# Performance work log

Measured on AMD Instinct MI355X. Metric: run time of the kernel, lower is better.

Reference implementation:

```python
import jax, jax.numpy as jnp
import numpy as np

ALPHA = 0.2  # LeakyReLU slope
S1, S2 = 5, 10  # neighbor sample sizes, hard-coded in the torch forward

N, F, D, C, B = 100000, 512, 256, 40, 16384


def setup_inputs() -> dict:
    key = jax.random.key(0)
    ks = jax.random.split(key, 7)
    x = jax.random.normal(ks[0], (N, F), dtype=jnp.float32)
    # xavier-like scaling for the weights
    W1 = jax.random.normal(ks[1], (D, F), dtype=jnp.float32) * (2.0 / (D + F)) ** 0.5
    W2 = jax.random.normal(ks[2], (D, D), dtype=jnp.float32) * (2.0 / (D + D)) ** 0.5
    Wc = jax.random.normal(ks[3], (C, D), dtype=jnp.float32) * (2.0 / (C + D)) ** 0.5
    nodes = jax.random.randint(ks[4], (B,), 0, N, dtype=jnp.int32)
    neigh1 = jax.random.randint(ks[5], (N, S1), 0, N, dtype=jnp.int32)
    neigh2 = jax.random.randint(ks[6], (B, S2), 0, N, dtype=jnp.int32)
    return {"x": x, "W1": W1, "W2": W2, "Wc": Wc,
            "nodes": nodes, "neigh1": neigh1, "neigh2": neigh2}


def leaky_relu(v):
    return jnp.where(v >= 0, v, ALPHA * v)


def reference(x, W1, W2, Wc, nodes, neigh1, neigh2):
    # Layer 1 (MeanAggregator, gcn=True): mean over sampled neighbors + self,
    # then linear transform + LeakyReLU. Computed for all N nodes.
    agg1 = (x[neigh1].sum(axis=1) + x) / (S1 + 1)          # [N, F]
    h1 = leaky_relu(agg1 @ W1.T)                            # [N, D]
    # Layer 2: mean over sampled neighbors + self, on batch nodes.
    agg2 = (h1[neigh2].sum(axis=1) + h1[nodes]) / (S2 + 1)  # [B, D]
    h2 = leaky_relu(agg2 @ W2.T)                            # [B, D]
    # scores = self.weight.mm(x_2.t()).t()
    scores = h2 @ Wc.T                                      # [B, C]
    return scores
```

## Files before the change

kernel.cpp:

```cpp
#include <hip/hip_runtime.h>
#include <hip/hip_bf16.h>


#define NN 100000
#define FF 512
#define DD 256
#define BB 16384
#define CC 40

typedef __attribute__((ext_vector_type(8))) short bf16x8;
typedef __attribute__((ext_vector_type(4))) float f32x4;
typedef unsigned short u16;
typedef unsigned int u32;

__device__ __forceinline__ float bf_lo(u32 u) { u32 v = u << 16; float f; __builtin_memcpy(&f, &v, 4); return f; }
__device__ __forceinline__ float bf_hi(u32 u) { u32 v = u & 0xffff0000u; float f; __builtin_memcpy(&f, &v, 4); return f; }
__device__ __forceinline__ float2 bf2f(u32 u) { return make_float2(bf_lo(u), bf_hi(u)); }
__device__ __forceinline__ u32 packbf2(float a, float b) {
  __hip_bfloat162 h = __float22bfloat162_rn(make_float2(a, b));
  u32 u; __builtin_memcpy(&u, &h, 4); return u;
}
__device__ __forceinline__ u16 fbits(float v) {
  __hip_bfloat16 h = __float2bfloat16(v);
  u16 u; __builtin_memcpy(&u, &h, 2); return u;
}
__device__ __forceinline__ float lrelu(float v) { return v >= 0.f ? v : 0.2f * v; }
__device__ __forceinline__ int swz(int r, int c) { return r * 128 + ((c ^ (r & 7)) << 4); }

__global__ __launch_bounds__(256) void k0_cvt(
    const float* __restrict__ W1, const float* __restrict__ W2, const float* __restrict__ Wc,
    u16* __restrict__ w1b, u16* __restrict__ w2b, u16* __restrict__ wcb)
{
  const int i = blockIdx.x * 256 + threadIdx.x;
  const float* src; u16* dst; int off;
  if (i < 32768)      { src = W1; dst = w1b; off = i * 4; }
  else if (i < 49152) { src = W2; dst = w2b; off = (i - 32768) * 4; }
  else if (i < 51712) { src = Wc; dst = wcb; off = (i - 49152) * 4; }
  else return;
  const float4 v = *(const float4*)(src + off);
  uint2 o; o.x = packbf2(v.x, v.y); o.y = packbf2(v.z, v.w);
  *(uint2*)(dst + off) = o;
}

__global__ __launch_bounds__(512) void k1_gemm(
    const float* __restrict__ x, const u16* __restrict__ w1b, u16* __restrict__ z)
{
  __shared__ __align__(16) unsigned char lds[49152];

  const int t = threadIdx.x;
  const int rowBase = blockIdx.x * 128;
  const int lane = t & 63, w = t >> 6;
  const int wm = w >> 2, wn = w & 3;
  const int lr = lane & 15, kg = lane >> 4;

  u32 offA[2]; int aW[2];
#pragma unroll
  for (int i = 0; i < 2; ++i) {
    const int id = t + i * 512;
    const int r = id >> 3, c = id & 7;
    int row = rowBase + r; if (row > NN - 1) row = NN - 1;
    offA[i] = (u32)row * FF + c * 8;
    aW[i] = swz(r, c);
  }
  u32 offB[4]; int bW[4];
#pragma unroll
  for (int i = 0; i < 4; ++i) {
    const int id = t + i * 512;
    const int r = id >> 3, c = id & 7;
    offB[i] = (u32)r * FF + c * 8;
    bW[i] = 16384 + swz(r, c);
  }
  int aA[2][4], bA[2][4];
#pragma unroll
  for (int kk = 0; kk < 2; ++kk) {
    const int cb = kk * 4 + kg;
#pragma unroll
    for (int m = 0; m < 4; ++m) aA[kk][m] = swz(wm * 64 + m * 16 + lr, cb);
#pragma unroll
    for (int n = 0; n < 4; ++n) bA[kk][n] = 16384 + swz(wn * 64 + n * 16 + lr, cb);
  }

  f32x4 acc[4][4];
#pragma unroll
  for (int m = 0; m < 4; ++m)
#pragma unroll
    for (int n = 0; n < 4; ++n) acc[m][n] = (f32x4)0.0f;

  for (int ks = 0; ks < 8; ++ks) {
    __syncthreads();
#pragma unroll
    for (int i = 0; i < 2; ++i) {
      const float4 v0 = *(const float4*)(x + offA[i] + ks * 64);
      const float4 v1 = *(const float4*)(x + offA[i] + ks * 64 + 4);
      uint4 o;
      o.x = packbf2(v0.x, v0.y); o.y = packbf2(v0.z, v0.w);
      o.z = packbf2(v1.x, v1.y); o.w = packbf2(v1.z, v1.w);
      *(uint4*)(lds + aW[i]) = o;
    }
#pragma unroll
    for (int i = 0; i < 4; ++i)
      *(uint4*)(lds + bW[i]) = *(const uint4*)(w1b + offB[i] + ks * 64);
    __syncthreads();
#pragma unroll
    for (int kk = 0; kk < 2; ++kk) {
      bf16x8 av[4], bv[4];
#pragma unroll
      for (int m = 0; m < 4; ++m) av[m] = *(const bf16x8*)(lds + aA[kk][m]);
#pragma unroll
      for (int n = 0; n < 4; ++n) bv[n] = *(const bf16x8*)(lds + bA[kk][n]);
#pragma unroll
      for (int m = 0; m < 4; ++m)
#pragma unroll
        for (int n = 0; n < 4; ++n)
          acc[m][n] = __builtin_amdgcn_mfma_f32_16x16x32_bf16(av[m], bv[n], acc[m][n], 0, 0, 0);
    }
  }
#pragma unroll
  for (int m = 0; m < 4; ++m) {
    const int r0 = rowBase + wm * 64 + m * 16 + kg * 4;
#pragma unroll
    for (int j = 0; j < 4; ++j)
#pragma unroll
      for (int n = 0; n < 4; ++n)
        z[(u32)(r0 + j) * DD + wn * 64 + n * 16 + lr] = fbits(acc[m][n][j]);
  }
}

__global__ __launch_bounds__(256) void k2_agg1(
    const u16* __restrict__ z, const int* __restrict__ neigh1, u16* __restrict__ h1)
{
  const int t = threadIdx.x;
  const int row = blockIdx.x * 8 + (t >> 5);
  const int ch = t & 31;
  const u32 o0 = (u32)row * DD + ch * 8;
  uint4 a = *(const uint4*)(z + o0);
  float2 s0 = bf2f(a.x), s1 = bf2f(a.y), s2 = bf2f(a.z), s3 = bf2f(a.w);
#pragma unroll
  for (int j = 0; j < 5; ++j) {
    const int idx = neigh1[row * 5 + j];
    const uint4 v = *(const uint4*)(z + (u32)idx * DD + ch * 8);
    s0.x += bf_lo(v.x); s0.y += bf_hi(v.x);
    s1.x += bf_lo(v.y); s1.y += bf_hi(v.y);
    s2.x += bf_lo(v.z); s2.y += bf_hi(v.z);
    s3.x += bf_lo(v.w); s3.y += bf_hi(v.w);
  }
  const float sc = 1.0f / 6.0f;
  uint4 o;
  o.x = packbf2(lrelu(s0.x * sc), lrelu(s0.y * sc));
  o.y = packbf2(lrelu(s1.x * sc), lrelu(s1.y * sc));
  o.z = packbf2(lrelu(s2.x * sc), lrelu(s2.y * sc));
  o.w = packbf2(lrelu(s3.x * sc), lrelu(s3.y * sc));
  *(uint4*)(h1 + o0) = o;
}

__global__ __launch_bounds__(256) void k3_agg_gemm(
    const u16* __restrict__ h1, const u16* __restrict__ w2b,
    const int* __restrict__ nodes, const int* __restrict__ neigh2,
    u16* __restrict__ h2)
{
  __shared__ __align__(16) unsigned char lds[8192 + 32768];

  const int t = threadIdx.x;
  const int rowBase = blockIdx.x * 64;
  const int lane = t & 63, w = t >> 6;
  const int lr = lane & 15, kg = lane >> 4;

  u32 offA[2][11]; int aW[2];
#pragma unroll
  for (int i = 0; i < 2; ++i) {
    const int id = t + i * 256;
    const int r = id >> 3, c = id & 7;
    const int b = rowBase + r;
    offA[i][0] = (u32)nodes[b] * DD + c * 8;
#pragma unroll
    for (int j = 0; j < 10; ++j)
      offA[i][1 + j] = (u32)neigh2[b * 10 + j] * DD + c * 8;
    aW[i] = swz(r, c);
  }
  u32 offB[8]; int bW[8];
#pragma unroll
  for (int i = 0; i < 8; ++i) {
    const int id = t + i * 256;
    const int r = id >> 3, c = id & 7;
    offB[i] = (u32)r * DD + c * 8;
    bW[i] = 8192 + swz(r, c);
  }
  int aA[2][4], bA[2][4];
#pragma unroll
  for (int kk = 0; kk < 2; ++kk) {
    const int cb = kk * 4 + kg;
#pragma unroll
    for (int m = 0; m < 4; ++m) aA[kk][m] = swz(m * 16 + lr, cb);
#pragma unroll
    for (int n = 0; n < 4; ++n) bA[kk][n] = 8192 + swz(w * 64 + n * 16 + lr, cb);
  }

  f32x4 acc[4][4];
#pragma unroll
  for (int m = 0; m < 4; ++m)
#pragma unroll
    for (int n = 0; n < 4; ++n) acc[m][n] = (f32x4)0.0f;

  for (int ks = 0; ks < 4; ++ks) {
    __syncthreads();
#pragma unroll
    for (int i = 0; i < 2; ++i) {
      float2 s0 = make_float2(0.f, 0.f), s1 = make_float2(0.f, 0.f);
      float2 s2 = make_float2(0.f, 0.f), s3 = make_float2(0.f, 0.f);
#pragma unroll
      for (int j = 0; j < 11; ++j) {
        const uint4 v = *(const uint4*)(h1 + offA[i][j] + ks * 64);
        s0.x += bf_lo(v.x); s0.y += bf_hi(v.x);
        s1.x += bf_lo(v.y); s1.y += bf_hi(v.y);
        s2.x += bf_lo(v.z); s2.y += bf_hi(v.z);
        s3.x += bf_lo(v.w); s3.y += bf_hi(v.w);
      }
      const float sc = 1.0f / 11.0f;
      uint4 o;
      o.x = packbf2(s0.x * sc, s0.y * sc);
      o.y = packbf2(s1.x * sc, s1.y * sc);
      o.z = packbf2(s2.x * sc, s2.y * sc);
      o.w = packbf2(s3.x * sc, s3.y * sc);
      *(uint4*)(lds + aW[i]) = o;
    }
#pragma unroll
    for (int i = 0; i < 8; ++i)
      *(uint4*)(lds + bW[i]) = *(const uint4*)(w2b + offB[i] + ks * 64);
    __syncthreads();
#pragma unroll
    for (int kk = 0; kk < 2; ++kk) {
      bf16x8 av[4], bv[4];
#pragma unroll
      for (int m = 0; m < 4; ++m) av[m] = *(const bf16x8*)(lds + aA[kk][m]);
#pragma unroll
      for (int n = 0; n < 4; ++n) bv[n] = *(const bf16x8*)(lds + bA[kk][n]);
#pragma unroll
      for (int m = 0; m < 4; ++m)
#pragma unroll
        for (int n = 0; n < 4; ++n)
          acc[m][n] = __builtin_amdgcn_mfma_f32_16x16x32_bf16(av[m], bv[n], acc[m][n], 0, 0, 0);
    }
  }
#pragma unroll
  for (int m = 0; m < 4; ++m) {
    const int r0 = rowBase + m * 16 + kg * 4;
#pragma unroll
    for (int j = 0; j < 4; ++j)
#pragma unroll
      for (int n = 0; n < 4; ++n)
        h2[(u32)(r0 + j) * DD + w * 64 + n * 16 + lr] = fbits(lrelu(acc[m][n][j]));
  }
}

__global__ __launch_bounds__(256) void k4_scores(
    const u16* __restrict__ h2, const u16* __restrict__ wcb, float* __restrict__ out)
{
  __shared__ __align__(16) unsigned char lds[8192 + 6144];

  const int t = threadIdx.x;
  const int rowBase = blockIdx.x * 64;
  const int lane = t & 63, w = t >> 6;
  const int lr = lane & 15, kg = lane >> 4;

  u32 offA[2]; int aW[2];
#pragma unroll
  for (int i = 0; i < 2; ++i) {
    const int id = t + i * 256;
    const int r = id >> 3, c = id & 7;
    offA[i] = (u32)(rowBase + r) * DD + c * 8;
    aW[i] = swz(r, c);
  }
  u32 offBc[2]; int bWr[2]; int bValid[2]; int bRow[2];
#pragma unroll
  for (int i = 0; i < 2; ++i) {
    const int id = t + i * 256;
    const int r = id >> 3, c = id & 7;
    bValid[i] = (id < 384);
    bRow[i] = r;
    offBc[i] = (u32)r * DD + c * 8;
    bWr[i] = 8192 + swz(r, c);
  }

  int aA[2], bA[2][3];
#pragma unroll
  for (int kk = 0; kk < 2; ++kk) {
    const int cb = kk * 4 + kg;
    aA[kk] = swz(w * 16 + lr, cb);
#pragma unroll
    for (int n = 0; n < 3; ++n) bA[kk][n] = 8192 + swz(n * 16 + lr, cb);
  }

  f32x4 acc[3];
#pragma unroll
  for (int n = 0; n < 3; ++n) acc[n] = (f32x4)0.0f;

  for (int ks = 0; ks < 4; ++ks) {
    __syncthreads();
#pragma unroll
    for (int i = 0; i < 2; ++i)
      *(uint4*)(lds + aW[i]) = *(const uint4*)(h2 + offA[i] + ks * 64);
#pragma unroll
    for (int i = 0; i < 2; ++i) {
      if (bValid[i]) {
        uint4 v = make_uint4(0u, 0u, 0u, 0u);
        if (bRow[i] < CC) v = *(const uint4*)(wcb + offBc[i] + ks * 64);
        *(uint4*)(lds + bWr[i]) = v;
      }
    }
    __syncthreads();
#pragma unroll
    for (int kk = 0; kk < 2; ++kk) {
      const bf16x8 a = *(const bf16x8*)(lds + aA[kk]);
#pragma unroll
      for (int n = 0; n < 3; ++n) {
        const bf16x8 b = *(const bf16x8*)(lds + bA[kk][n]);
        acc[n] = __builtin_amdgcn_mfma_f32_16x16x32_bf16(a, b, acc[n], 0, 0, 0);
      }
    }
  }
#pragma unroll
  for (int n = 0; n < 3; ++n) {
    const int col = n * 16 + lr;
    if (col < CC) {
#pragma unroll
      for (int j = 0; j < 4; ++j) {
        const int r = rowBase + w * 16 + kg * 4 + j;
        out[(u32)r * CC + col] = acc[n][j];
      }
    }
  }
}

extern "C" void kernel_launch(void* const* d_in, const int* in_sizes, int n_in,
                              void* d_out, int out_size, void* d_ws, size_t ws_size,
                              hipStream_t stream) {
  const float* x      = (const float*)d_in[0];
  const float* W1     = (const float*)d_in[1];
  const float* W2     = (const float*)d_in[2];
  const float* Wc     = (const float*)d_in[3];
  const int* nodes    = (const int*)d_in[4];
  const int* neigh1   = (const int*)d_in[5];
  const int* neigh2   = (const int*)d_in[6];

  u16* z   = (u16*)d_ws;
  u16* h1  = z  + (size_t)100096 * 256;
  u16* h2  = h1 + (size_t)100096 * 256;
  u16* w1b = h2 + (size_t)16384 * 256;
  u16* w2b = w1b + (size_t)256 * 512;
  u16* wcb = w2b + (size_t)256 * 256;

  k0_cvt<<<dim3(202), dim3(256), 0, stream>>>(W1, W2, Wc, w1b, w2b, wcb);
  k1_gemm<<<dim3(782), dim3(512), 0, stream>>>(x, w1b, z);
  k2_agg1<<<dim3(12500), dim3(256), 0, stream>>>(z, neigh1, h1);
  k3_agg_gemm<<<dim3(256), dim3(256), 0, stream>>>(h1, w2b, nodes, neigh2, h2);
  k4_scores<<<dim3(256), dim3(256), 0, stream>>>(h2, wcb, (float*)d_out);
}
```

Measured before the change: 157.5 us.

## Fuse layer-2 GEMM with score GEMM, prefetch A tiles, async LDS weight loads

Merges the layer-2 aggregation GEMM and the classifier GEMM into one kernel, so h2 stays in LDS and is never written to or re-read from global memory. The weights are pre-swizzled during the bf16 conversion so they can go straight into LDS through global_load_lds. In k1 and the fused kernel, the next k-step's x or h1 gather loads are issued before the MFMA work so their latency overlaps compute. The fused kernel uses 512-thread blocks with a larger LDS footprint, which may lower occupancy.

```diff
diff --git a/kernel.cpp b/kernel.cpp
--- a/kernel.cpp
+++ b/kernel.cpp
@@ -26,23 +26,32 @@
 }
 __device__ __forceinline__ float lrelu(float v) { return v >= 0.f ? v : 0.2f * v; }
 __device__ __forceinline__ int swz(int r, int c) { return r * 128 + ((c ^ (r & 7)) << 4); }
+__device__ __forceinline__ void gld_lds16(const u16* g, void* l) {
+  __builtin_amdgcn_global_load_lds((const __attribute__((address_space(1))) unsigned int*)g,
+                                   (__attribute__((address_space(3))) unsigned int*)l, 16, 0, 0);
+}
 
 __global__ __launch_bounds__(256) void k0_cvt(
     const float* __restrict__ W1, const float* __restrict__ W2, const float* __restrict__ Wc,
     u16* __restrict__ w1b, u16* __restrict__ w2b, u16* __restrict__ wcb)
 {
   const int i = blockIdx.x * 256 + threadIdx.x;
-  const float* src; u16* dst; int off;
-  if (i < 32768)      { src = W1; dst = w1b; off = i * 4; }
-  else if (i < 49152) { src = W2; dst = w2b; off = (i - 32768) * 4; }
-  else if (i < 51712) { src = Wc; dst = wcb; off = (i - 49152) * 4; }
+  const float* src; u16* dst; int r, cc, rowE;
+  if (i < 16384)      { src = W1; dst = w1b; r = i >> 6; cc = i & 63; rowE = 512; }
+  else if (i < 24576) { int j = i - 16384; src = W2; dst = w2b; r = j >> 5; cc = j & 31; rowE = 256; }
+  else if (i < 25856) { int j = i - 24576; src = Wc; dst = wcb; r = j >> 5; cc = j & 31; rowE = 256; }
   else return;
-  const float4 v = *(const float4*)(src + off);
-  uint2 o; o.x = packbf2(v.x, v.y); o.y = packbf2(v.z, v.w);
-  *(uint2*)(dst + off) = o;
-}
-
-__global__ __launch_bounds__(512) void k1_gemm(
+  const int g = cc >> 3, cp = cc & 7;
+  const float* s = src + (u32)r * rowE + g * 64 + (u32)(cp ^ (r & 7)) * 8;
+  const float4 v0 = *(const float4*)s;
+  const float4 v1 = *(const float4*)(s + 4);
+  uint4 o;
+  o.x = packbf2(v0.x, v0.y); o.y = packbf2(v0.z, v0.w);
+  o.z = packbf2(v1.x, v1.y); o.w = packbf2(v1.z, v1.w);
+  *(uint4*)(dst + (u32)r * rowE + g * 64 + cp * 8) = o;
+}
+
+__global__ __launch_bounds__(512, 4) void k1_gemm(
     const float* __restrict__ x, const u16* __restrict__ w1b, u16* __restrict__ z)
 {
   __shared__ __align__(16) unsigned char lds[49152];
@@ -62,14 +71,9 @@
     offA[i] = (u32)row * FF + c * 8;
     aW[i] = swz(r, c);
   }
-  u32 offB[4]; int bW[4];
-#pragma unroll
-  for (int i = 0; i < 4; ++i) {
-    const int id = t + i * 512;
-    const int r = id >> 3, c = id & 7;
-    offB[i] = (u32)r * FF + c * 8;
-    bW[i] = 16384 + swz(r, c);
-  }
+  const u32 bofs = (u32)(w * 8 + (lane >> 3)) * FF + (u32)(lane & 7) * 8;
+  unsigned char* bl0 = lds + 16384 + w * 1024;
+
   int aA[2][4], bA[2][4];
 #pragma unroll
   for (int kk = 0; kk < 2; ++kk) {
@@ -86,21 +90,34 @@
 #pragma unroll
     for (int n = 0; n < 4; ++n) acc[m][n] = (f32x4)0.0f;
 
+  float4 pa[2][2];
+#pragma unroll
+  for (int i = 0; i < 2; ++i) {
+    pa[i][0] = *(const float4*)(x + offA[i]);
+    pa[i][1] = *(const float4*)(x + offA[i] + 4);
+  }
+
   for (int ks = 0; ks < 8; ++ks) {
+    if (ks) __builtin_amdgcn_s_barrier();
+#pragma unroll
+    for (int i = 0; i < 2; ++i) {
+      uint4 o;
+      o.x = packbf2(pa[i][0].x, pa[i][0].y); o.y = packbf2(pa[i][0].z, pa[i][0].w);
+      o.z = packbf2(pa[i][1].x, pa[i][1].y); o.w = packbf2(pa[i][1].z, pa[i][1].w);
+      *(uint4*)(lds + aW[i]) = o;
+    }
+#pragma unroll
+    for (int i = 0; i < 4; ++i)
+      gld_lds16(w1b + bofs + (u32)i * 64 * FF + (u32)ks * 64, bl0 + i * 8192);
     __syncthreads();
-#pragma unroll
-    for (int i = 0; i < 2; ++i) {
-      const float4 v0 = *(const float4*)(x + offA[i] + ks * 64);
-      const float4 v1 = *(const float4*)(x + offA[i] + ks * 64 + 4);
-      uint4 o;
-      o.x = packbf2(v0.x, v0.y); o.y = packbf2(v0.z, v0.w);
-      o.z = packbf2(v1.x, v1.y); o.w = packbf2(v1.z, v1.w);
-      *(uint4*)(lds + aW[i]) = o;
-    }
-#pragma unroll
-    for (int i = 0; i < 4; ++i)
-      *(uint4*)(lds + bW[i]) = *(const uint4*)(w1b + offB[i] + ks * 64);
-    __syncthreads();
+    if (ks < 7) {
+#pragma unroll
+      for (int i = 0; i < 2; ++i) {
+        pa[i][0] = *(const float4*)(x + offA[i] + (u32)(ks + 1) * 64);
+        pa[i][1] = *(const float4*)(x + offA[i] + (u32)(ks + 1) * 64 + 4);
+      }
+    }
+    __builtin_amdgcn_sched_barrier(0);
 #pragma unroll
     for (int kk = 0; kk < 2; ++kk) {
       bf16x8 av[4], bv[4];
@@ -153,67 +170,69 @@
   *(uint4*)(h1 + o0) = o;
 }
 
-__global__ __launch_bounds__(256) void k3_agg_gemm(
-    const u16* __restrict__ h1, const u16* __restrict__ w2b,
-    const int* __restrict__ nodes, const int* __restrict__ neigh2,
-    u16* __restrict__ h2)
+__global__ __launch_bounds__(512, 2) void k3_fused(
+    const u16* __restrict__ h1, const u16* __restrict__ w2b, const u16* __restrict__ wcb,
+    const int* __restrict__ nodes, const int* __restrict__ neigh2, float* __restrict__ out)
 {
-  __shared__ __align__(16) unsigned char lds[8192 + 32768];
+  __shared__ __align__(16) unsigned char lds[65536];
 
   const int t = threadIdx.x;
   const int rowBase = blockIdx.x * 64;
   const int lane = t & 63, w = t >> 6;
+  const int wm = w >> 2, wn = w & 3;
   const int lr = lane & 15, kg = lane >> 4;
 
-  u32 offA[2][11]; int aW[2];
-#pragma unroll
-  for (int i = 0; i < 2; ++i) {
-    const int id = t + i * 256;
-    const int r = id >> 3, c = id & 7;
-    const int b = rowBase + r;
-    offA[i][0] = (u32)nodes[b] * DD + c * 8;
-#pragma unroll
-    for (int j = 0; j < 10; ++j)
-      offA[i][1 + j] = (u32)neigh2[b * 10 + j] * DD + c * 8;
-    aW[i] = swz(r, c);
-  }
-  u32 offB[8]; int bW[8];
-#pragma unroll
-  for (int i = 0; i < 8; ++i) {
-    const int id = t + i * 256;
-    const int r = id >> 3, c = id & 7;
-    offB[i] = (u32)r * DD + c * 8;
-    bW[i] = 8192 + swz(r, c);
-  }
-  int aA[2][4], bA[2][4];
+#pragma unroll
+  for (int i = 0; i < 3; ++i) {
+    const int id = t + i * 512;
+    uint4 v = make_uint4(0u, 0u, 0u, 0u);
+    if (id < 1280) v = *(const uint4*)(wcb + (u32)id * 8);
+    *(uint4*)(lds + 40960 + id * 16) = v;
+  }
+
+  const int r = t >> 3, c = t & 7;
+  const int b = rowBase + r;
+  u32 offA[11];
+  offA[0] = (u32)nodes[b] * DD + (u32)c * 8;
+#pragma unroll
+  for (int j = 0; j < 10; ++j)
+    offA[1 + j] = (u32)neigh2[b * 10 + j] * DD + (u32)c * 8;
+  const int aW = swz(r, c);
+
+  const u32 bofs = (u32)(w * 8 + (lane >> 3)) * DD + (u32)(lane & 7) * 8;
+  unsigned char* bl0 = lds + 8192 + w * 1024;
+
+  int aA[2][2], bA[2][4];
 #pragma unroll
   for (int kk = 0; kk < 2; ++kk) {
     const int cb = kk * 4 + kg;
 #pragma unroll
-    for (int m = 0; m < 4; ++m) aA[kk][m] = swz(m * 16 + lr, cb);
-#pragma unroll
-    for (int n = 0; n < 4; ++n) bA[kk][n] = 8192 + swz(w * 64 + n * 16 + lr, cb);
-  }
-
-  f32x4 acc[4][4];
-#pragma unroll
-  for (int m = 0; m < 4; ++m)
+    for (int m = 0; m < 2; ++m) aA[kk][m] = swz(wm * 32 + m * 16 + lr, cb);
+#pragma unroll
+    for (int n = 0; n < 4; ++n) bA[kk][n] = 8192 + swz(wn * 64 + n * 16 + lr, cb);
+  }
+
+  f32x4 acc[2][4];
+#pragma unroll
+  for (int m = 0; m < 2; ++m)
 #pragma unroll
     for (int n = 0; n < 4; ++n) acc[m][n] = (f32x4)0.0f;
 
+  uint4 ag[11];
+#pragma unroll
+  for (int j = 0; j < 11; ++j) ag[j] = *(const uint4*)(h1 + offA[j]);
+
   for (int ks = 0; ks < 4; ++ks) {
-    __syncthreads();
-#pragma unroll
-    for (int i = 0; i < 2; ++i) {
+    if (ks) __builtin_amdgcn_s_barrier();
+    {
       float2 s0 = make_float2(0.f, 0.f), s1 = make_float2(0.f, 0.f);
       float2 s2 = make_float2(0.f, 0.f), s3 = make_float2(0.f, 0.f);
 #pragma unroll
       for (int j = 0; j < 11; ++j) {
-        const uint4 v = *(const uint4*)(h1 + offA[i][j] + ks * 64);
-        s0.x += bf_lo(v.x); s0.y += bf_hi(v.x);
-        s1.x += bf_lo(v.y); s1.y += bf_hi(v.y);
-        s2.x += bf_lo(v.z); s2.y += bf_hi(v.z);
-        s3.x += bf_lo(v.w); s3.y += bf_hi(v.w);
+        s0.x += bf_lo(ag[j].x); s0.y += bf_hi(ag[j].x);
+        s1.x += bf_lo(ag[j].y); s1.y += bf_hi(ag[j].y);
+        s2.x += bf_lo(ag[j].z); s2.y += bf_hi(ag[j].z);
+        s3.x += bf_lo(ag[j].w); s3.y += bf_hi(ag[j].w);
       }
       const float sc = 1.0f / 11.0f;
       uint4 o;
@@ -221,111 +240,77 @@
       o.y = packbf2(s1.x * sc, s1.y * sc);
       o.z = packbf2(s2.x * sc, s2.y * sc);
       o.w = packbf2(s3.x * sc, s3.y * sc);
-      *(uint4*)(lds + aW[i]) = o;
-    }
-#pragma unroll
-    for (int i = 0; i < 8; ++i)
-      *(uint4*)(lds + bW[i]) = *(const uint4*)(w2b + offB[i] + ks * 64);
+      *(uint4*)(lds + aW) = o;
+    }
+#pragma unroll
+    for (int i = 0; i < 4; ++i)
+      gld_lds16(w2b + bofs + (u32)i * 64 * DD + (u32)ks * 64, bl0 + i * 8192);
     __syncthreads();
+    if (ks < 3) {
+#pragma unroll
+      for (int j = 0; j < 11; ++j)
+        ag[j] = *(const uint4*)(h1 + offA[j] + (u32)(ks + 1) * 64);
+    }
+    __builtin_amdgcn_sched_barrier(0);
 #pragma unroll
     for (int kk = 0; kk < 2; ++kk) {
-      bf16x8 av[4], bv[4];
-#pragma unroll
-      for (int m = 0; m < 4; ++m) av[m] = *(const bf16x8*)(lds + aA[kk][m]);
+      bf16x8 av[2], bv[4];
+#pragma unroll
+      for (int m = 0; m < 2; ++m) av[m] = *(const bf16x8*)(lds + aA[kk][m]);
 #pragma unroll
       for (int n = 0; n < 4; ++n) bv[n] = *(const bf16x8*)(lds + bA[kk][n]);
 #pragma unroll
-      for (int m = 0; m < 4; ++m)
+      for (int m = 0; m < 2; ++m)
 #pragma unroll
         for (int n = 0; n < 4; ++n)
           acc[m][n] = __builtin_amdgcn_mfma_f32_16x16x32_bf16(av[m], bv[n], acc[m][n], 0, 0, 0);
     }
   }
-#pragma unroll
-  for (int m = 0; m < 4; ++m) {
-    const int r0 = rowBase + m * 16 + kg * 4;
-#pragma unroll
-    for (int j = 0; j < 4; ++j)
-#pragma unroll
-      for (int n = 0; n < 4; ++n)
-        h2[(u32)(r0 + j) * DD + w * 64 + n * 16 + lr] = fbits(lrelu(acc[m][n][j]));
-  }
-}
-
-__global__ __launch_bounds__(256) void k4_scores(
-    const u16* __restrict__ h2, const u16* __restrict__ wcb, float* __restrict__ out)
-{
-  __shared__ __align__(16) unsigned char lds[8192 + 6144];
-
-  const int t = threadIdx.x;
-  const int rowBase = blockIdx.x * 64;
-  const int lane = t & 63, w = t >> 6;
-  const int lr = lane & 15, kg = lane >> 4;
-
-  u32 offA[2]; int aW[2];
-#pragma unroll
-  for (int i = 0; i < 2; ++i) {
-    const int id = t + i * 256;
-    const int r = id >> 3, c = id & 7;
-    offA[i] = (u32)(rowBase + r) * DD + c * 8;
-    aW[i] = swz(r, c);
-  }
-  u32 offBc[2]; int bWr[2]; int bValid[2]; int bRow[2];
-#pragma unroll
-  for (int i = 0; i < 2; ++i) {
-    const int id = t + i * 256;
-    const int r = id >> 3, c = id & 7;
-    bValid[i] = (id < 384);
-    bRow[i] = r;
-    offBc[i] = (u32)r * DD + c * 8;
-    bWr[i] = 8192 + swz(r, c);
-  }
-
-  int aA[2], bA[2][3];
-#pragma unroll
-  for (int kk = 0; kk < 2; ++kk) {
-    const int cb = kk * 4 + kg;
-    aA[kk] = swz(w * 16 + lr, cb);
-#pragma unroll
-    for (int n = 0; n < 3; ++n) bA[kk][n] = 8192 + swz(n * 16 + lr, cb);
-  }
-
-  f32x4 acc[3];
-#pragma unroll
-  for (int n = 0; n < 3; ++n) acc[n] = (f32x4)0.0f;
-
-  for (int ks = 0; ks < 4; ++ks) {
-    __syncthreads();
-#pragma unroll
-    for (int i = 0; i < 2; ++i)
-      *(uint4*)(lds + aW[i]) = *(const uint4*)(h2 + offA[i] + ks * 64);
-#pragma unroll
-    for (int i = 0; i < 2; ++i) {
-      if (bValid[i]) {
-        uint4 v = make_uint4(0u, 0u, 0u, 0u);
-        if (bRow[i] < CC) v = *(const uint4*)(wcb + offBc[i] + ks * 64);
-        *(uint4*)(lds + bWr[i]) = v;
-      }
-    }
-    __syncthreads();
-#pragma unroll
-    for (int kk = 0; kk < 2; ++kk) {
-      const bf16x8 a = *(const bf16x8*)(lds + aA[kk]);
+
+  __syncthreads();
+#pragma unroll
+  for (int m = 0; m < 2; ++m) {
+#pragma unroll
+    for (int j = 0; j < 4; ++j) {
+      const int row = wm * 32 + m * 16 + kg * 4 + j;
+#pragma unroll
+      for (int n = 0; n < 4; ++n) {
+        const int col = wn * 64 + n * 16 + lr;
+        const int ch = col >> 3;
+        const int pch = (ch & 24) | ((ch ^ row) & 7);
+        *(u16*)(lds + row * 512 + pch * 16 + (col & 7) * 2) = fbits(lrelu(acc[m][n][j]));
+      }
+    }
+  }
+  __syncthreads();
+
+  if (w < 4) {
+    f32x4 acc2[3];
+#pragma unroll
+    for (int n = 0; n < 3; ++n) acc2[n] = (f32x4)0.0f;
+    const int arow = w * 16 + lr;
+#pragma unroll
+    for (int ks2 = 0; ks2 < 8; ++ks2) {
+      const int chb = ks2 * 4 + kg;
+      const int pchA = (chb & 24) | ((chb ^ arow) & 7);
+      const bf16x8 a = *(const bf16x8*)(lds + arow * 512 + pchA * 16);
 #pragma unroll
       for (int n = 0; n < 3; ++n) {
-        const bf16x8 b = *(const bf16x8*)(lds + bA[kk][n]);
-        acc[n] = __builtin_amdgcn_mfma_f32_16x16x32_bf16(a, b, acc[n], 0, 0, 0);
-      }
-    }
-  }
-#pragma unroll
-  for (int n = 0; n < 3; ++n) {
-    const int col = n * 16 + lr;
-    if (col < CC) {
-#pragma unroll
-      for (int j = 0; j < 4; ++j) {
-        const int r = rowBase + w * 16 + kg * 4 + j;
-        out[(u32)r * CC + col] = acc[n][j];
+        const int brow = n * 16 + lr;
+        const int pchB = (chb & 24) | ((chb ^ brow) & 7);
+        const bf16x8 bb = *(const bf16x8*)(lds + 40960 + brow * 512 + pchB * 16);
+        acc2[n] = __builtin_amdgcn_mfma_f32_16x16x32_bf16(a, bb, acc2[n], 0, 0, 0);
+      }
+    }
+#pragma unroll
+    for (int n = 0; n < 3; ++n) {
+      const int col = n * 16 + lr;
+      if (col < CC) {
+#pragma unroll
+        for (int j = 0; j < 4; ++j) {
+          const int rr = rowBase + w * 16 + kg * 4 + j;
+          out[(u32)rr * CC + col] = acc2[n][j];
+        }
       }
     }
   }
@@ -334,24 +319,22 @@
 extern "C" void kernel_launch(void* const* d_in, const int* in_sizes, int n_in,
                               void* d_out, int out_size, void* d_ws, size_t ws_size,
                               hipStream_t stream) {
-  const float* x      = (const float*)d_in[0];
-  const float* W1     = (const float*)d_in[1];
-  const float* W2     = (const float*)d_in[2];
-  const float* Wc     = (const float*)d_in[3];
-  const int* nodes    = (const int*)d_in[4];
-  const int* neigh1   = (const int*)d_in[5];
-  const int* neigh2   = (const int*)d_in[6];
+  const float* x    = (const float*)d_in[0];
+  const float* W1   = (const float*)d_in[1];
+  const float* W2   = (const float*)d_in[2];
+  const float* Wc   = (const float*)d_in[3];
+  const int* nodes  = (const int*)d_in[4];
+  const int* neigh1 = (const int*)d_in[5];
+  const int* neigh2 = (const int*)d_in[6];
 
   u16* z   = (u16*)d_ws;
-  u16* h1  = z  + (size_t)100096 * 256;
-  u16* h2  = h1 + (size_t)100096 * 256;
-  u16* w1b = h2 + (size_t)16384 * 256;
+  u16* h1  = z + (size_t)100096 * 256;
+  u16* w1b = h1 + (size_t)100096 * 256;
   u16* w2b = w1b + (size_t)256 * 512;
   u16* wcb = w2b + (size_t)256 * 256;
 
-  k0_cvt<<<dim3(202), dim3(256), 0, stream>>>(W1, W2, Wc, w1b, w2b, wcb);
+  k0_cvt<<<dim3(101), dim3(256), 0, stream>>>(W1, W2, Wc, w1b, w2b, wcb);
   k1_gemm<<<dim3(782), dim3(512), 0, stream>>>(x, w1b, z);
   k2_agg1<<<dim3(12500), dim3(256), 0, stream>>>(z, neigh1, h1);
-  k3_agg_gemm<<<dim3(256), dim3(256), 0, stream>>>(h1, w2b, nodes, neigh2, h2);
-  k4_scores<<<dim3(256), dim3(256), 0, stream>>>(h2, wcb, (float*)d_out);
-}
+  k3_fused<<<dim3(256), dim3(512), 0, stream>>>(h1, w2b, wcb, nodes, neigh2, (float*)d_out);
+}
```

New measurement: 154.5 us. No clear change (-1.9%).
